# Kernel optimization log

Measured on AMD Instinct MI355X. Metric: run time of the kernel, lower is better.

## Reference

```python
import jax, jax.numpy as jnp
import numpy as np

SPECTRAL_RADIUS = 0.95
EPS = 1e-8


def _get_UV(U, V, spectral_radius):
    """Spectrally normalized low-rank factors (3-step power iteration)."""
    dim = U.shape[0]
    UV = U @ V  # [D, D]
    UVc = jax.lax.stop_gradient(UV)  # power iteration is no_grad in torch
    # fixed random start vector (torch uses randn; fixed seed for determinism)
    u = jnp.asarray(np.random.default_rng(0).standard_normal(dim), dtype=U.dtype)
    u = u / jnp.linalg.norm(u)
    v = None
    for _ in range(3):
        v = UVc.T @ u
        v = v / (jnp.linalg.norm(v) + EPS)
        u = UVc @ v
        u = u / (jnp.linalg.norm(u) + EPS)
    sigma = jnp.abs(u @ UV @ v)  # grad flows through UV here
    scale = spectral_radius / (sigma + EPS)
    s = jnp.sqrt(scale)
    return U * s, V * s


def setup_inputs() -> dict:
    key = jax.random.key(0)
    ks = jax.random.split(key, 5)
    T, B, D, R = 1024, 32, 1024, 64
    x = jax.random.normal(ks[0], (T, B, D), dtype=jnp.float32)
    z = jax.random.normal(ks[1], (T, B, D), dtype=jnp.float32)
    h0 = jnp.zeros((B, D), dtype=jnp.float32)
    # xavier-uniform-ish W_x
    lim = (6.0 / (D + D)) ** 0.5
    W_x = jax.random.uniform(ks[2], (D, D), minval=-lim, maxval=lim, dtype=jnp.float32)
    U = jax.random.normal(ks[3], (D, R), dtype=jnp.float32) * 0.3 / (D ** 0.5)
    V = jax.random.normal(ks[4], (R, D), dtype=jnp.float32) * 0.3 / (D ** 0.5)
    b = jnp.zeros((D,), dtype=jnp.float32)
    return {"x": x, "z": z, "h0": h0, "W_x": W_x, "U": U, "V": V, "b": b}


def reference(x, z, h0, W_x, U, V, b):
    Un, Vn = _get_UV(U, V, SPECTRAL_RADIUS)
    # precompute input projection for all steps: [T, B, D]
    xW = jnp.einsum('tbd,ed->tbe', x, W_x) + b
    silu_z = jax.nn.silu(z)

    def step(h_prev, inputs):
        xw_t, sz_t = inputs
        # low-rank recurrence: (h @ V^T) @ U^T
        h_new = jnp.tanh(xw_t + (h_prev @ Vn.T) @ Un.T)
        out = h_new * sz_t
        return h_new, (h_new, out)

    _, (hs, outs) = jax.lax.scan(step, h0, (xW, silu_z))
    h_all = jnp.concatenate([h0[None], hs], axis=0)  # [T+1, B, D]
    return outs, h_all
```

## Files before the change

kernel.cpp:

```cpp
#include <hip/hip_runtime.h>
#include <cstdint>
#include <cstddef>

typedef unsigned int u32;
typedef unsigned long long u64;
typedef __uint128_t u128;

#define TT 1024
#define BB 32
#define DDIM 1024
#define RRANK 64
#define BD (BB*DDIM)
#define TBD (TT*BB*DDIM)

constexpr double kLN2 = 0.6931471805599453094172321214581766;

constexpr double cexp_(double x){
  int k = (int)(x / kLN2 + (x >= 0.0 ? 0.5 : -0.5));
  double r = x - (double)k * kLN2;
  double term = 1.0, sum = 1.0;
  for (int n = 1; n <= 26; ++n){ term *= r / (double)n; sum += term; }
  double p = 1.0; int kk = k;
  while (kk > 0){ p *= 2.0; --kk; }
  while (kk < 0){ p *= 0.5; ++kk; }
  return sum * p;
}
constexpr double clog_(double x){
  int e = 0; double m = x;
  while (m >= 1.3348398541700344) { m *= 0.5; ++e; }
  while (m <  0.6674199270850172) { m *= 2.0; --e; }
  double s = (m - 1.0) / (m + 1.0);
  double s2 = s * s, term = s, sum = 0.0;
  for (int n = 0; n < 20; ++n){ sum += term / (double)(2*n+1); term *= s2; }
  return 2.0 * sum + (double)e * kLN2;
}
constexpr double csqrt_(double x){
  double g = 0.5 * (x + 1.0);
  for (int i = 0; i < 40; ++i) g = 0.5 * (g + x / g);
  return g;
}

constexpr double ZIG_R    = 3.6541528853610087963519472518;
constexpr double ZIG_INVR = 0.27366123732975827203338247596;
constexpr double ZIG_V    = 4.92867323399e-3;

struct ZigT { u64 ki[256]; double wi[256]; double fi[256]; };

constexpr ZigT make_zig(){
  ZigT t{};
  const double m1 = 4503599627370496.0;
  double dn = ZIG_R, tn = ZIG_R;
  const double vn = ZIG_V;
  const double q = vn / cexp_(-0.5 * dn * dn);
  t.ki[0] = (u64)((dn / q) * m1);
  t.ki[1] = 0;
  t.wi[0] = q / m1;
  t.wi[255] = dn / m1;
  t.fi[0] = 1.0;
  t.fi[255] = cexp_(-0.5 * dn * dn);
  for (int i = 254; i >= 1; --i){
    dn = csqrt_(-2.0 * clog_(vn / dn + cexp_(-0.5 * dn * dn)));
    t.ki[i+1] = (u64)((dn / tn) * m1);
    tn = dn;
    t.fi[i] = cexp_(-0.5 * dn * dn);
    t.wi[i] = dn / m1;
  }
  return t;
}

__device__ const ZigT ZT = make_zig();

__device__ __forceinline__ float block_sum_1024(float v, float* buf, int tid){
  buf[tid] = v; __syncthreads();
  #pragma unroll 1
  for (int s = 512; s > 0; s >>= 1){
    if (tid < s) buf[tid] += buf[tid + s];
    __syncthreads();
  }
  float r = buf[0];
  __syncthreads();
  return r;
}

__global__ __launch_bounds__(1024) void k1_spectral(const float* __restrict__ U,
    const float* __restrict__ V, float* __restrict__ wsp){
  __shared__ float u_sh[1024];
  __shared__ float v_sh[1024];
  __shared__ float part[1024];
  __shared__ float t_sh[64];
  __shared__ float s_sh[64];
  __shared__ u64 ki_s[256];
  __shared__ double wi_s[256];
  __shared__ double fi_s[256];
  const int tid = threadIdx.x;
  if (tid < 256){ ki_s[tid] = ZT.ki[tid]; wi_s[tid] = ZT.wi[tid]; fi_s[tid] = ZT.fi[tid]; }
  __syncthreads();

  if (tid == 0){
    u32 hc = 0x43b0d7e5u;
    u32 pool[4];
    for (int i = 0; i < 4; ++i){
      u32 v = 0u;
      v ^= hc; hc *= 0x931e8875u; v *= hc; v ^= v >> 16;
      pool[i] = v;
    }
    for (int s = 0; s < 4; ++s){
      for (int d = 0; d < 4; ++d){
        if (s == d) continue;
        u32 v = pool[s];
        v ^= hc; hc *= 0x931e8875u; v *= hc; v ^= v >> 16;
        u32 r = 0xca01f9ddu * pool[d] - 0x4973f715u * v;
        r ^= r >> 16;
        pool[d] = r;
      }
    }
    u32 ghc = 0x8b51f9ddu;
    u32 st32[8];
    for (int i = 0; i < 8; ++i){
      u32 dv = pool[i & 3];
      dv ^= ghc; ghc *= 0x58f38dedu; dv *= ghc; dv ^= dv >> 16;
      st32[i] = dv;
    }
    u64 sd0 = (u64)st32[0] | ((u64)st32[1] << 32);
    u64 sd1 = (u64)st32[2] | ((u64)st32[3] << 32);
    u64 sd2 = (u64)st32[4] | ((u64)st32[5] << 32);
    u64 sd3 = (u64)st32[6] | ((u64)st32[7] << 32);
    const u128 MULT = ((u128)2549297995355413924ULL << 64) | (u128)4865540595714422341ULL;
    u128 initstate = ((u128)sd0 << 64) | (u128)sd1;
    u128 initseq   = ((u128)sd2 << 64) | (u128)sd3;
    u128 state = 0;
    u128 inc = (initseq << 1) | (u128)1;
    state = state * MULT + inc;
    state += initstate;
    state = state * MULT + inc;
    int filled = 0;
    while (filled < 1024){
      state = state * MULT + inc;
      u64 hi = (u64)(state >> 64), lo = (u64)state;
      u32 rot = (u32)(state >> 122);
      u64 ru = hi ^ lo;
      ru = (ru >> rot) | (ru << ((64u - rot) & 63u));
      int idx = (int)(ru & 0xff);
      u64 r9 = ru >> 8;
      int sgn = (int)(r9 & 1);
      u64 rabs = (r9 >> 1) & 0x000fffffffffffffULL;
      double x = (double)rabs * wi_s[idx];
      if (sgn) x = -x;
      if (rabs < ki_s[idx]){ u_sh[filled++] = (float)x; continue; }
      if (idx == 0){
        for (;;){
          state = state * MULT + inc;
          u64 h1 = (u64)(state>>64), l1 = (u64)state; u32 ro1 = (u32)(state>>122);
          u64 a = h1 ^ l1; a = (a>>ro1)|(a<<((64u-ro1)&63u));
          double ua = (double)(a >> 11) * (1.0/9007199254740992.0);
          state = state * MULT + inc;
          u64 h2 = (u64)(state>>64), l2 = (u64)state; u32 ro2 = (u32)(state>>122);
          u64 bd = h2 ^ l2; bd = (bd>>ro2)|(bd<<((64u-ro2)&63u));
          double ub = (double)(bd >> 11) * (1.0/9007199254740992.0);
          double xt = -ZIG_INVR * log1p(-ua);
          double yt = -log1p(-ub);
          if (yt + yt > xt * xt){
            double val = ((rabs >> 8) & 1) ? -(ZIG_R + xt) : (ZIG_R + xt);
            u_sh[filled++] = (float)val;
            break;
          }
        }
        continue;
      }
      state = state * MULT + inc;
      u64 h3 = (u64)(state>>64), l3 = (u64)state; u32 ro3 = (u32)(state>>122);
      u64 c = h3 ^ l3; c = (c>>ro3)|(c<<((64u-ro3)&63u));
      double uc = (double)(c >> 11) * (1.0/9007199254740992.0);
      if ((fi_s[idx-1] - fi_s[idx]) * uc + fi_s[idx] < exp(-0.5 * x * x)){
        u_sh[filled++] = (float)x;
      }
    }
  }
  __syncthreads();

  float uv = u_sh[tid];
  float ss = block_sum_1024(uv * uv, part, tid);
  float nrm = sqrtf(ss);
  u_sh[tid] = uv / nrm;
  __syncthreads();

  for (int it = 0; it < 3; ++it){
    {
      const int r = tid & 63, g = tid >> 6;
      float p = 0.f;
      for (int j = 0; j < 64; ++j) p += U[(size_t)(g*64+j)*64 + r] * u_sh[g*64+j];
      part[tid] = p;
    }
    __syncthreads();
    if (tid < 64){ float s = 0.f; for (int g = 0; g < 16; ++g) s += part[g*64+tid]; t_sh[tid] = s; }
    __syncthreads();
    float vvv = 0.f;
    for (int r = 0; r < 64; ++r) vvv += V[(size_t)r*1024 + tid] * t_sh[r];
    float nv = sqrtf(block_sum_1024(vvv*vvv, part, tid)) + 1e-8f;
    vvv /= nv;
    v_sh[tid] = vvv;
    __syncthreads();
    {
      const int r = tid & 63, g = tid >> 6;
      float p = 0.f;
      for (int j = 0; j < 64; ++j) p += V[(size_t)r*1024 + g*64 + j] * v_sh[g*64+j];
      part[tid] = p;
    }
    __syncthreads();
    if (tid < 64){ float s = 0.f; for (int g = 0; g < 16; ++g) s += part[g*64+tid]; s_sh[tid] = s; }
    __syncthreads();
    float uuu = 0.f;
    for (int r = 0; r < 64; ++r) uuu += U[(size_t)tid*64 + r] * s_sh[r];
    float nu = sqrtf(block_sum_1024(uuu*uuu, part, tid)) + 1e-8f;
    uuu /= nu;
    u_sh[tid] = uuu;
    __syncthreads();
  }
  {
    const int r = tid & 63, g = tid >> 6;
    float p = 0.f;
    for (int j = 0; j < 64; ++j) p += U[(size_t)(g*64+j)*64 + r] * u_sh[g*64+j];
    part[tid] = p;
  }
  __syncthreads();
  if (tid < 64){ float s = 0.f; for (int g = 0; g < 16; ++g) s += part[g*64+tid]; t_sh[tid] = s; }
  __syncthreads();
  if (tid == 0){
    float sig = 0.f;
    for (int r = 0; r < 64; ++r) sig += t_sh[r] * s_sh[r];
    sig = fabsf(sig);
    wsp[0] = 0.95f / (sig + 1e-8f);
  }
}

__global__ __launch_bounds__(256) void k2_gemm(const float* __restrict__ X,
    const float* __restrict__ W, const float* __restrict__ bvec,
    float* __restrict__ C){
  __shared__ float As[16][132];
  __shared__ float Ws[16][68];
  const int bm = blockIdx.y * 128;
  const int bn = blockIdx.x * 64;
  const int tid = (int)threadIdx.x;
  const int tx = tid & 15;
  const int ty = tid >> 4;
  const int lm = tid >> 2;
  const int lk = (tid & 3) * 4;
  float acc[8][4];
  #pragma unroll
  for (int i = 0; i < 8; ++i)
    #pragma unroll
    for (int j = 0; j < 4; ++j) acc[i][j] = 0.f;

  #pragma unroll 1
  for (int k0 = 0; k0 < 1024; k0 += 16){
    float4 a0 = *(const float4*)(X + (size_t)(bm+lm)*1024 + k0 + lk);
    float4 a1 = *(const float4*)(X + (size_t)(bm+64+lm)*1024 + k0 + lk);
    float4 w0 = *(const float4*)(W + (size_t)(bn+lm)*1024 + k0 + lk);
    As[lk+0][lm] = a0.x; As[lk+1][lm] = a0.y; As[lk+2][lm] = a0.z; As[lk+3][lm] = a0.w;
    As[lk+0][64+lm] = a1.x; As[lk+1][64+lm] = a1.y; As[lk+2][64+lm] = a1.z; As[lk+3][64+lm] = a1.w;
    Ws[lk+0][lm] = w0.x; Ws[lk+1][lm] = w0.y; Ws[lk+2][lm] = w0.z; Ws[lk+3][lm] = w0.w;
    __syncthreads();
    #pragma unroll
    for (int k = 0; k < 16; ++k){
      float4 av0 = *(const float4*)&As[k][ty*8];
      float4 av1 = *(const float4*)&As[k][ty*8+4];
      float4 wv  = *(const float4*)&Ws[k][tx*4];
      const float am[8] = {av0.x,av0.y,av0.z,av0.w,av1.x,av1.y,av1.z,av1.w};
      const float wn[4] = {wv.x,wv.y,wv.z,wv.w};
      #pragma unroll
      for (int i = 0; i < 8; ++i)
        #pragma unroll
        for (int j = 0; j < 4; ++j) acc[i][j] += am[i]*wn[j];
    }
    __syncthreads();
  }
  const float4 bv = *(const float4*)(bvec + bn + tx*4);
  #pragma unroll
  for (int i = 0; i < 8; ++i){
    const int row = bm + ty*8 + i;
    float4 o;
    o.x = acc[i][0] + bv.x;
    o.y = acc[i][1] + bv.y;
    o.z = acc[i][2] + bv.z;
    o.w = acc[i][3] + bv.w;
    *(float4*)(C + (size_t)row*1024 + bn + tx*4) = o;
  }
}

__global__ __launch_bounds__(1024) void k3_recur(const float* __restrict__ U,
    const float* __restrict__ V, const float* __restrict__ h0,
    const float* __restrict__ wsp, float* __restrict__ hall){
  __shared__ float h_sh[1024];
  __shared__ float part[1024];
  __shared__ __align__(16) float tmp_sh[64];
  __shared__ __align__(16) float VB[32768];
  const int tid = (int)threadIdx.x;
  const int lane = tid & 63;
  const int wv = tid >> 6;
  const int b = (int)blockIdx.x;
  const float scale = wsp[0];

  {
    const int r = tid >> 4, c = tid & 15;
    const float* src = V + (size_t)r*1024 + c*64 + 32;
    float* dst = VB + r*512 + c*32;
    #pragma unroll
    for (int g = 0; g < 8; ++g){
      float4 v4 = *(const float4*)(src + g*4);
      *(float4*)(dst + (((g ^ (r & 7))) << 2)) = v4;
    }
  }
  float vregA[32];
  #pragma unroll
  for (int q = 0; q < 8; ++q){
    float4 t4 = *(const float4*)(V + (size_t)lane*1024 + wv*64 + q*4);
    vregA[q*4+0]=t4.x; vregA[q*4+1]=t4.y; vregA[q*4+2]=t4.z; vregA[q*4+3]=t4.w;
  }
  float ureg[64];
  #pragma unroll
  for (int q = 0; q < 16; ++q){
    float4 t4 = *(const float4*)(U + (size_t)tid*64 + q*4);
    ureg[q*4+0]=t4.x; ureg[q*4+1]=t4.y; ureg[q*4+2]=t4.z; ureg[q*4+3]=t4.w;
  }
  const float* vb_lane = VB + lane*512 + wv*32;
  const int r7 = lane & 7;

  float h = h0[b*1024 + tid];
  h_sh[tid] = h;
  float* base = hall + BD + (size_t)b*1024 + tid;
  float xwv = base[0];
  __syncthreads();

  #pragma unroll 1
  for (int t = 0; t < TT; ++t){
    const int tn = (t < TT-1) ? t+1 : t;
    const float xw_next = base[(size_t)tn*BD];

    float p = 0.f, p2 = 0.f;
    #pragma unroll
    for (int q = 0; q < 8; ++q){
      float4 h4 = *(const float4*)(h_sh + wv*64 + q*4);
      p  = fmaf(h4.x, vregA[q*4+0], p);
      p2 = fmaf(h4.y, vregA[q*4+1], p2);
      p  = fmaf(h4.z, vregA[q*4+2], p);
      p2 = fmaf(h4.w, vregA[q*4+3], p2);
    }
    #pragma unroll
    for (int q = 0; q < 8; ++q){
      float4 h4 = *(const float4*)(h_sh + wv*64 + 32 + q*4);
      float4 v4 = *(const float4*)(vb_lane + ((q ^ r7) << 2));
      p  = fmaf(h4.x, v4.x, p);
      p2 = fmaf(h4.y, v4.y, p2);
      p  = fmaf(h4.z, v4.z, p);
      p2 = fmaf(h4.w, v4.w, p2);
    }
    part[tid] = p + p2;
    __syncthreads();
    if (tid < 64){
      float s = 0.f;
      #pragma unroll
      for (int g = 0; g < 16; ++g) s += part[g*64 + tid];
      tmp_sh[tid] = s * scale;
    }
    __syncthreads();
    float a0 = 0.f, a1 = 0.f;
    #pragma unroll
    for (int q = 0; q < 16; ++q){
      float4 t4 = *(const float4*)(tmp_sh + q*4);
      a0 = fmaf(t4.x, ureg[q*4+0], a0);
      a1 = fmaf(t4.y, ureg[q*4+1], a1);
      a0 = fmaf(t4.z, ureg[q*4+2], a0);
      a1 = fmaf(t4.w, ureg[q*4+3], a1);
    }
    h = tanhf(xwv + a0 + a1);
    base[(size_t)t*BD] = h;
    h_sh[tid] = h;
    xwv = xw_next;
  }
}

__global__ __launch_bounds__(256) void k4_out(const float* __restrict__ z,
    const float* __restrict__ h0, float* __restrict__ dout){
  const int i = (int)(blockIdx.x * blockDim.x + threadIdx.x);
  const float4 zv = *((const float4*)z + i);
  const float4 hv = *((const float4*)(dout + TBD + BD) + i);
  float4 o;
  o.x = hv.x * (zv.x / (1.f + expf(-zv.x)));
  o.y = hv.y * (zv.y / (1.f + expf(-zv.y)));
  o.z = hv.z * (zv.z / (1.f + expf(-zv.z)));
  o.w = hv.w * (zv.w / (1.f + expf(-zv.w)));
  *((float4*)dout + i) = o;
  if (i < BD/4){
    *((float4*)(dout + TBD) + i) = *((const float4*)h0 + i);
  }
}

extern "C" void kernel_launch(void* const* d_in, const int* in_sizes, int n_in,
                              void* d_out, int out_size, void* d_ws, size_t ws_size,
                              hipStream_t stream) {
  (void)in_sizes; (void)n_in; (void)out_size; (void)ws_size;
  const float* x    = (const float*)d_in[0];
  const float* z    = (const float*)d_in[1];
  const float* h0   = (const float*)d_in[2];
  const float* Wx   = (const float*)d_in[3];
  const float* U    = (const float*)d_in[4];
  const float* V    = (const float*)d_in[5];
  const float* bias = (const float*)d_in[6];
  float* outp = (float*)d_out;
  float* hall = outp + (size_t)TBD;
  float* wsp  = (float*)d_ws;

  k1_spectral<<<1, 1024, 0, stream>>>(U, V, wsp);
  dim3 g2(1024/64, 32768/128);
  k2_gemm<<<g2, 256, 0, stream>>>(x, Wx, bias, hall + BD);
  k3_recur<<<BB, 1024, 0, stream>>>(U, V, h0, wsp, hall);
  k4_out<<<TBD/4/256, 256, 0, stream>>>(z, h0, outp);
}
```

Baseline: 3.997 ms.

## Halve recurrence block to 512 threads, two hidden units per thread

The recurrent kernel now runs 512 threads per batch row instead of 1024, and each thread handles two hidden elements. Each wave now covers 64 h-elements for the V projection instead of 32: half of V stays in registers and the other half sits in a transposed shared-memory layout with no XOR swizzle. The goal is to cut the partial-sum reduction work (8 partials instead of 16) and the cost of block-wide barriers. The trade-off is higher register pressure (64 V values plus 128 U values per thread) and more serial FMA work per thread on the latency-bound critical path.

```diff
diff --git a/kernel.cpp b/kernel.cpp
--- a/kernel.cpp
+++ b/kernel.cpp
@@ -287,13 +287,13 @@
   }
 }
 
-__global__ __launch_bounds__(1024) void k3_recur(const float* __restrict__ U,
+__global__ __launch_bounds__(512, 2) void k3_recur(const float* __restrict__ U,
     const float* __restrict__ V, const float* __restrict__ h0,
     const float* __restrict__ wsp, float* __restrict__ hall){
   __shared__ float h_sh[1024];
-  __shared__ float part[1024];
+  __shared__ float part[512];
   __shared__ __align__(16) float tmp_sh[64];
-  __shared__ __align__(16) float VB[32768];
+  __shared__ __align__(16) float VBt[32768];
   const int tid = (int)threadIdx.x;
   const int lane = tid & 63;
   const int wv = tid >> 6;
@@ -301,54 +301,59 @@
   const float scale = wsp[0];
 
   {
-    const int r = tid >> 4, c = tid & 15;
-    const float* src = V + (size_t)r*1024 + c*64 + 32;
-    float* dst = VB + r*512 + c*32;
-    #pragma unroll
-    for (int g = 0; g < 8; ++g){
-      float4 v4 = *(const float4*)(src + g*4);
-      *(float4*)(dst + (((g ^ (r & 7))) << 2)) = v4;
-    }
-  }
-  float vregA[32];
+    const float* vsrc = V + (size_t)lane*1024 + 512 + wv*64;
+    #pragma unroll
+    for (int q = 0; q < 16; ++q){
+      float4 v4 = *(const float4*)(vsrc + q*4);
+      *(float4*)(VBt + (size_t)((wv*16 + q)*64 + lane)*4) = v4;
+    }
+  }
+  float vreg[64];
   #pragma unroll
-  for (int q = 0; q < 8; ++q){
+  for (int q = 0; q < 16; ++q){
     float4 t4 = *(const float4*)(V + (size_t)lane*1024 + wv*64 + q*4);
-    vregA[q*4+0]=t4.x; vregA[q*4+1]=t4.y; vregA[q*4+2]=t4.z; vregA[q*4+3]=t4.w;
-  }
-  float ureg[64];
+    vreg[q*4+0]=t4.x; vreg[q*4+1]=t4.y; vreg[q*4+2]=t4.z; vreg[q*4+3]=t4.w;
+  }
+  float ureg0[64], ureg1[64];
   #pragma unroll
   for (int q = 0; q < 16; ++q){
     float4 t4 = *(const float4*)(U + (size_t)tid*64 + q*4);
-    ureg[q*4+0]=t4.x; ureg[q*4+1]=t4.y; ureg[q*4+2]=t4.z; ureg[q*4+3]=t4.w;
-  }
-  const float* vb_lane = VB + lane*512 + wv*32;
-  const int r7 = lane & 7;
-
-  float h = h0[b*1024 + tid];
+    ureg0[q*4+0]=t4.x; ureg0[q*4+1]=t4.y; ureg0[q*4+2]=t4.z; ureg0[q*4+3]=t4.w;
+  }
+  #pragma unroll
+  for (int q = 0; q < 16; ++q){
+    float4 t4 = *(const float4*)(U + (size_t)(tid+512)*64 + q*4);
+    ureg1[q*4+0]=t4.x; ureg1[q*4+1]=t4.y; ureg1[q*4+2]=t4.z; ureg1[q*4+3]=t4.w;
+  }
+
+  float h  = h0[b*1024 + tid];
+  float h2 = h0[b*1024 + tid + 512];
   h_sh[tid] = h;
+  h_sh[tid + 512] = h2;
   float* base = hall + BD + (size_t)b*1024 + tid;
-  float xwv = base[0];
+  float xw0 = base[0];
+  float xw1 = base[512];
   __syncthreads();
 
   #pragma unroll 1
   for (int t = 0; t < TT; ++t){
     const int tn = (t < TT-1) ? t+1 : t;
-    const float xw_next = base[(size_t)tn*BD];
+    const float nx0 = base[(size_t)tn*BD];
+    const float nx1 = base[(size_t)tn*BD + 512];
 
     float p = 0.f, p2 = 0.f;
     #pragma unroll
-    for (int q = 0; q < 8; ++q){
+    for (int q = 0; q < 16; ++q){
       float4 h4 = *(const float4*)(h_sh + wv*64 + q*4);
-      p  = fmaf(h4.x, vregA[q*4+0], p);
-      p2 = fmaf(h4.y, vregA[q*4+1], p2);
-      p  = fmaf(h4.z, vregA[q*4+2], p);
-      p2 = fmaf(h4.w, vregA[q*4+3], p2);
-    }
-    #pragma unroll
-    for (int q = 0; q < 8; ++q){
-      float4 h4 = *(const float4*)(h_sh + wv*64 + 32 + q*4);
-      float4 v4 = *(const float4*)(vb_lane + ((q ^ r7) << 2));
+      p  = fmaf(h4.x, vreg[q*4+0], p);
+      p2 = fmaf(h4.y, vreg[q*4+1], p2);
+      p  = fmaf(h4.z, vreg[q*4+2], p);
+      p2 = fmaf(h4.w, vreg[q*4+3], p2);
+    }
+    #pragma unroll
+    for (int q = 0; q < 16; ++q){
+      float4 h4 = *(const float4*)(h_sh + 512 + wv*64 + q*4);
+      float4 v4 = *(const float4*)(VBt + (size_t)((wv*16 + q)*64 + lane)*4);
       p  = fmaf(h4.x, v4.x, p);
       p2 = fmaf(h4.y, v4.y, p2);
       p  = fmaf(h4.z, v4.z, p);
@@ -359,23 +364,30 @@
     if (tid < 64){
       float s = 0.f;
       #pragma unroll
-      for (int g = 0; g < 16; ++g) s += part[g*64 + tid];
+      for (int g = 0; g < 8; ++g) s += part[g*64 + tid];
       tmp_sh[tid] = s * scale;
     }
     __syncthreads();
-    float a0 = 0.f, a1 = 0.f;
+    float a0 = 0.f, a1 = 0.f, b0 = 0.f, b1 = 0.f;
     #pragma unroll
     for (int q = 0; q < 16; ++q){
       float4 t4 = *(const float4*)(tmp_sh + q*4);
-      a0 = fmaf(t4.x, ureg[q*4+0], a0);
-      a1 = fmaf(t4.y, ureg[q*4+1], a1);
-      a0 = fmaf(t4.z, ureg[q*4+2], a0);
-      a1 = fmaf(t4.w, ureg[q*4+3], a1);
-    }
-    h = tanhf(xwv + a0 + a1);
+      a0 = fmaf(t4.x, ureg0[q*4+0], a0);
+      a1 = fmaf(t4.y, ureg0[q*4+1], a1);
+      a0 = fmaf(t4.z, ureg0[q*4+2], a0);
+      a1 = fmaf(t4.w, ureg0[q*4+3], a1);
+      b0 = fmaf(t4.x, ureg1[q*4+0], b0);
+      b1 = fmaf(t4.y, ureg1[q*4+1], b1);
+      b0 = fmaf(t4.z, ureg1[q*4+2], b0);
+      b1 = fmaf(t4.w, ureg1[q*4+3], b1);
+    }
+    h  = tanhf(xw0 + a0 + a1);
+    h2 = tanhf(xw1 + b0 + b1);
     base[(size_t)t*BD] = h;
+    base[(size_t)t*BD + 512] = h2;
     h_sh[tid] = h;
-    xwv = xw_next;
+    h_sh[tid + 512] = h2;
+    xw0 = nx0; xw1 = nx1;
   }
 }
 
@@ -413,6 +425,6 @@
   k1_spectral<<<1, 1024, 0, stream>>>(U, V, wsp);
   dim3 g2(1024/64, 32768/128);
   k2_gemm<<<g2, 256, 0, stream>>>(x, Wx, bias, hall + BD);
-  k3_recur<<<BB, 1024, 0, stream>>>(U, V, h0, wsp, hall);
+  k3_recur<<<BB, 512, 0, stream>>>(U, V, h0, wsp, hall);
   k4_out<<<TBD/4/256, 256, 0, stream>>>(z, h0, outp);
 }
```

Measured after the change: 4.228 ms. +5.8%, slower.
